# Performance work log

Hardware: AMD Instinct MI355X
Metric: run time of the kernel (lower is better)

Reference implementation:

```python
import jax, jax.numpy as jnp
import numpy as np

N_NODES = 100000
N_EDGES = 6400000
NODE_IN = 128
HID = 64


def _mlp(x, w1, b1, w2, b2):
    # Linear -> ReLU -> Linear -> ReLU
    return jax.nn.relu(jax.nn.relu(x @ w1 + b1) @ w2 + b2)


def _edge_softmax_agg(node_h, logits, src, dst, n):
    # DGL edge_softmax: softmax of edge logits over incoming edges per dst node,
    # then weighted sum of src node features scattered to dst.
    m = jax.lax.stop_gradient(jax.ops.segment_max(logits, dst, num_segments=n))
    e = jnp.exp(logits - m[dst])
    s = jax.ops.segment_sum(e, dst, num_segments=n)
    w = e / s[dst]
    return jax.ops.segment_sum(w * node_h[src], dst, num_segments=n)


def setup_inputs() -> dict:
    key = jax.random.key(0)
    ks = jax.random.split(key, 24)
    d = {
        "node_feat": jax.random.normal(ks[0], (N_NODES, NODE_IN), jnp.float32),
        "edge_feat": jax.random.normal(ks[1], (N_EDGES, 1), jnp.float32),
        "edge_dist": jax.random.normal(ks[2], (N_EDGES, 1), jnp.float32),
        "src": jax.random.randint(ks[3], (N_EDGES,), 0, N_NODES, jnp.int32),
        "dst": jax.random.randint(ks[4], (N_EDGES,), 0, N_NODES, jnp.int32),
    }
    def lin(k, fin, fout):
        kw, kb = jax.random.split(k)
        return (jax.random.normal(kw, (fin, fout), jnp.float32) / np.sqrt(fin),
                jax.random.normal(kb, (fout,), jnp.float32) * 0.01)
    d["enc_w1"], d["enc_b1"] = lin(ks[5], NODE_IN, HID)
    d["enc_w2"], d["enc_b2"] = lin(ks[6], HID, 1)
    d["nu_w1"], d["nu_b1"] = lin(ks[7], 2, HID)
    d["nu_w2"], d["nu_b2"] = lin(ks[8], HID, 1)
    d["eu_w1"], d["eu_b1"] = lin(ks[9], 3, HID)
    d["eu_w2"], d["eu_b2"] = lin(ks[10], HID, 1)
    d["dec_w1"], d["dec_b1"] = lin(ks[11], 1, HID)
    d["dec_w2"], d["dec_b2"] = lin(ks[12], HID, 1)
    return d


def reference(node_feat, edge_feat, edge_dist, src, dst,
              enc_w1, enc_b1, enc_w2, enc_b2,
              nu_w1, nu_b1, nu_w2, nu_b2,
              eu_w1, eu_b1, eu_w2, eu_b2,
              dec_w1, dec_b1, dec_w2, dec_b2):
    n = node_feat.shape[0]
    # encoder on raw node features -> [N,1]
    h = _mlp(node_feat, enc_w1, enc_b1, enc_w2, enc_b2)
    # softmax aggregation weighted by edge 'dist'
    h = _edge_softmax_agg(h, edge_dist, src, dst, n)
    # edge update: concat([edge_feat, src_h, dst_h]) -> MLP -> [E,1]
    eh = _mlp(jnp.concatenate([edge_feat, h[src], h[dst]], axis=-1),
              eu_w1, eu_b1, eu_w2, eu_b2)
    # pull: sum incoming updated edge features per dst node
    agg = jax.ops.segment_sum(eh, dst, num_segments=n)
    # node update: concat([agg_m, h]) -> MLP -> [N,1]
    h = _mlp(jnp.concatenate([agg, h], axis=-1), nu_w1, nu_b1, nu_w2, nu_b2)
    # second softmax aggregation with updated edge features as logits
    h2 = _edge_softmax_agg(h, eh, src, dst, n)
    # decoder -> [N,1]
    return _mlp(h2, dec_w1, dec_b1, dec_w2, dec_b2)
```

## Files before the change

### kernel.cpp

```cpp
#include <hip/hip_runtime.h>


#define NHB 256

typedef int   iv4 __attribute__((ext_vector_type(4)));
typedef float fv4 __attribute__((ext_vector_type(4)));
typedef float fv2 __attribute__((ext_vector_type(2)));


__global__ void __launch_bounds__(256) k_chist(
    const int* __restrict__ DST, int* __restrict__ hist,
    int e, int nbkt, int shift, int epb)
{
    __shared__ int lh[512];
    for (int c = threadIdx.x; c < nbkt; c += blockDim.x) lh[c] = 0;
    __syncthreads();
    int b = blockIdx.x;
    int i0 = b * epb, i1 = min(i0 + epb, e);
    int nq = (i1 > i0) ? ((i1 - i0) >> 2) : 0;
    const iv4* D4 = reinterpret_cast<const iv4*>(DST + i0);
    for (int q = threadIdx.x; q < nq; q += blockDim.x) {
        iv4 d = D4[q];
        atomicAdd(&lh[d.x >> shift], 1);
        atomicAdd(&lh[d.y >> shift], 1);
        atomicAdd(&lh[d.z >> shift], 1);
        atomicAdd(&lh[d.w >> shift], 1);
    }
    for (int i = i0 + 4 * nq + threadIdx.x; i < i1; i += blockDim.x)
        atomicAdd(&lh[DST[i] >> shift], 1);
    __syncthreads();
    for (int c = threadIdx.x; c < nbkt; c += blockDim.x)
        hist[(size_t)c * NHB + b] = lh[c];
}

__global__ void __launch_bounds__(256) k_scanA(
    int* __restrict__ hist, int* __restrict__ bktCnt)
{
    int c = blockIdx.x;
    int* row = hist + (size_t)c * NHB;
    __shared__ int part[256];
    int t = threadIdx.x;
    int v = row[t];
    part[t] = v;
    __syncthreads();
    for (int off = 1; off < 256; off <<= 1) {
        int x = 0;
        if (t >= off) x = part[t - off];
        __syncthreads();
        part[t] += x;
        __syncthreads();
    }
    if (t == 255) bktCnt[c] = part[255];
    row[t] = part[t] - v;
}

__global__ void __launch_bounds__(256) k_scanB(
    const int* __restrict__ bktCnt, int* __restrict__ base, int nbkt, int e)
{
    __shared__ int part[256];
    int t = threadIdx.x;
    int v[4];
    int sum = 0;
    #pragma unroll
    for (int u = 0; u < 4; ++u) {
        int idx = t * 4 + u;
        v[u] = (idx < nbkt) ? bktCnt[idx] : 0;
        sum += v[u];
    }
    part[t] = sum;
    __syncthreads();
    for (int off = 1; off < 256; off <<= 1) {
        int x = 0;
        if (t >= off) x = part[t - off];
        __syncthreads();
        part[t] += x;
        __syncthreads();
    }
    int run = (t == 0) ? 0 : part[t - 1];
    #pragma unroll
    for (int u = 0; u < 4; ++u) {
        int idx = t * 4 + u;
        if (idx < nbkt) base[idx] = run;
        run += v[u];
    }
    if (t == 0) base[nbkt] = e;
}

__global__ void __launch_bounds__(256) k_scatter(
    const int* __restrict__ DST, const int* __restrict__ SRC,
    const float* __restrict__ DIST, const float* __restrict__ EF,
    const int* __restrict__ hist, const int* __restrict__ base,
    float2* __restrict__ payA, float* __restrict__ ef_s,
    int e, int nbkt, int shift, int epb)
{
    __shared__ int loff[512];
    int b = blockIdx.x;
    for (int c = threadIdx.x; c < nbkt; c += blockDim.x)
        loff[c] = base[c] + hist[(size_t)c * NHB + b];
    __syncthreads();
    int i0 = b * epb, i1 = min(i0 + epb, e);
    if (i0 >= i1) return;
    int mask = (1 << shift) - 1;
    int nq = (i1 - i0) >> 2;
    const iv4* D4 = reinterpret_cast<const iv4*>(DST + i0);
    const iv4* S4 = reinterpret_cast<const iv4*>(SRC + i0);
    const fv4* T4 = reinterpret_cast<const fv4*>(DIST + i0);
    const fv4* F4 = reinterpret_cast<const fv4*>(EF + i0);
    for (int q = threadIdx.x; q < nq; q += blockDim.x) {
        iv4 dv = __builtin_nontemporal_load(D4 + q);
        iv4 sv = __builtin_nontemporal_load(S4 + q);
        fv4 tv = __builtin_nontemporal_load(T4 + q);
        fv4 fv = __builtin_nontemporal_load(F4 + q);
        #pragma unroll
        for (int u = 0; u < 4; ++u) {
            int d = dv[u];
            int c = d >> shift;
            int pos = atomicAdd(&loff[c], 1);
            int sd = (sv[u] << shift) | (d & mask);
            payA[pos] = make_float2(__int_as_float(sd), tv[u]);
            ef_s[pos] = fv[u];
        }
    }
    for (int i = i0 + 4 * nq + threadIdx.x; i < i1; i += blockDim.x) {
        int d = DST[i];
        int c = d >> shift;
        int pos = atomicAdd(&loff[c], 1);
        int sd = (SRC[i] << shift) | (d & mask);
        payA[pos] = make_float2(__int_as_float(sd), DIST[i]);
        ef_s[pos] = EF[i];
    }
}


__global__ void __launch_bounds__(256) k_enc(
    const float* __restrict__ X, const float* __restrict__ W1,
    const float* __restrict__ B1, const float* __restrict__ W2,
    const float* __restrict__ B2, float* __restrict__ H0, int n)
{
    __shared__ float4 w1s[2048];
    for (int t = threadIdx.x; t < 2048; t += blockDim.x)
        w1s[t] = reinterpret_cast<const float4*>(W1)[t];
    __syncthreads();

    int i = blockIdx.x * blockDim.x + threadIdx.x;
    if (i >= n) return;

    const float4* xp = reinterpret_cast<const float4*>(X) + (size_t)i * 32;

    float acc[64];
    #pragma unroll
    for (int j = 0; j < 64; ++j) acc[j] = B1[j];

    for (int k4 = 0; k4 < 32; ++k4) {
        float4 xv = xp[k4];
        #pragma unroll
        for (int kk = 0; kk < 4; ++kk) {
            float x = (&xv.x)[kk];
            const float4* wrow = &w1s[(k4 * 4 + kk) * 16];
            #pragma unroll
            for (int j4 = 0; j4 < 16; ++j4) {
                float4 w = wrow[j4];
                acc[j4*4+0] = fmaf(x, w.x, acc[j4*4+0]);
                acc[j4*4+1] = fmaf(x, w.y, acc[j4*4+1]);
                acc[j4*4+2] = fmaf(x, w.z, acc[j4*4+2]);
                acc[j4*4+3] = fmaf(x, w.w, acc[j4*4+3]);
            }
        }
    }
    float o = B2[0];
    #pragma unroll
    for (int j = 0; j < 64; ++j)
        o = fmaf(fmaxf(acc[j], 0.f), W2[j], o);
    H0[i] = fmaxf(o, 0.f);
}


__global__ void __launch_bounds__(256) k_passA(
    const float2* __restrict__ payA, const float* __restrict__ H0,
    const int* __restrict__ base,
    float* __restrict__ pSum, float* __restrict__ pNum, int shift, int G)
{
    __shared__ float lsum[512], lnum[512];
    int c = blockIdx.x / G, g = blockIdx.x % G;
    int bw = 1 << shift, mask = bw - 1;
    for (int t = threadIdx.x; t < bw; t += blockDim.x) { lsum[t] = 0.f; lnum[t] = 0.f; }
    __syncthreads();
    int b0 = base[c], len = base[c + 1] - b0;
    int i0 = b0 + (int)(((long long)len * g) / G);
    int i1 = b0 + (int)(((long long)len * (g + 1)) / G);
    for (int i = i0 + threadIdx.x; i < i1; i += blockDim.x) {
        fv2 pa = __builtin_nontemporal_load(
            reinterpret_cast<const fv2*>(payA) + i);
        int sd = __float_as_int(pa.x);
        float ev = __expf(pa.y);
        atomicAdd(&lsum[sd & mask], ev);
        atomicAdd(&lnum[sd & mask], ev * H0[sd >> shift]);
    }
    __syncthreads();
    size_t po = (size_t)blockIdx.x << shift;
    for (int t = threadIdx.x; t < bw; t += blockDim.x) {
        pSum[po + t] = lsum[t];
        pNum[po + t] = lnum[t];
    }
}

__global__ void __launch_bounds__(256) k_finA(
    const float* __restrict__ pSum, const float* __restrict__ pNum,
    float* __restrict__ H1, int shift, int n, int G)
{
    int d = blockIdx.x * blockDim.x + threadIdx.x;
    if (d >= n) return;
    int c = d >> shift, t = d & ((1 << shift) - 1);
    size_t b = (size_t)c * G << shift;
    int bw = 1 << shift;
    float s = 0.f, m = 0.f;
    for (int g = 0; g < G; ++g) {
        s += pSum[b + (size_t)g * bw + t];
        m += pNum[b + (size_t)g * bw + t];
    }
    H1[d] = (s != 0.f) ? m / s : 0.f;
}

__global__ void __launch_bounds__(256) k_passB(
    const float2* __restrict__ payA, float* __restrict__ ef_s,
    const float* __restrict__ H1,
    const float* __restrict__ W1, const float* __restrict__ B1,
    const float* __restrict__ W2, const float* __restrict__ B2,
    const int* __restrict__ base,
    float* __restrict__ pAgg, float* __restrict__ pS2, int shift, int n, int G)
{
    __shared__ float h1loc[512], lagg[512], ls2[512];
    int bw = 1 << shift, mask = bw - 1;
    int c = blockIdx.x / G, g = blockIdx.x % G;
    int d0 = c << shift;
    for (int t = threadIdx.x; t < bw; t += blockDim.x) {
        int d = d0 + t;
        h1loc[t] = (d < n) ? H1[d] : 0.f;
        lagg[t] = 0.f;
        ls2[t] = 0.f;
    }
    __syncthreads();
    const float b2 = B2[0];
    int b0 = base[c], len = base[c + 1] - b0;
    int i0 = b0 + (int)(((long long)len * g) / G);
    int i1 = b0 + (int)(((long long)len * (g + 1)) / G);
    const int T = blockDim.x;
    for (int i = i0 + (int)threadIdx.x; i < i1; i += 4 * T) {
        float x0[4], hs[4], hd[4], o[4];
        int lo[4], pos[4];
        bool val[4];
        #pragma unroll
        for (int u = 0; u < 4; ++u) {
            int j = i + u * T;
            val[u] = (j < i1);
            pos[u] = j;
            if (val[u]) {
                fv2 pa = __builtin_nontemporal_load(
                    reinterpret_cast<const fv2*>(payA) + j);
                int sd = __float_as_int(pa.x);
                lo[u] = sd & mask;
                x0[u] = __builtin_nontemporal_load(ef_s + j);
                hs[u] = H1[sd >> shift];
                hd[u] = h1loc[lo[u]];
            } else { lo[u] = 0; x0[u] = 0.f; hs[u] = 0.f; hd[u] = 0.f; }
            o[u] = b2;
        }
        #pragma unroll 4
        for (int j = 0; j < 64; ++j) {
            float aj = W1[j], bj = W1[64 + j], cj = W1[128 + j];
            float dj = B1[j], vj = W2[j];
            #pragma unroll
            for (int u = 0; u < 4; ++u) {
                float t0 = fmaf(x0[u], aj, fmaf(hs[u], bj, fmaf(hd[u], cj, dj)));
                o[u] = fmaf(fmaxf(t0, 0.f), vj, o[u]);
            }
        }
        #pragma unroll
        for (int u = 0; u < 4; ++u) {
            if (val[u]) {
                float eh = fmaxf(o[u], 0.f);
                float ex = __expf(eh);
                ef_s[pos[u]] = ex;
                atomicAdd(&lagg[lo[u]], eh);
                atomicAdd(&ls2[lo[u]], ex);
            }
        }
    }
    __syncthreads();
    size_t po = (size_t)blockIdx.x << shift;
    for (int t = threadIdx.x; t < bw; t += blockDim.x) {
        pAgg[po + t] = lagg[t];
        pS2[po + t] = ls2[t];
    }
}

__global__ void __launch_bounds__(256) k_finB(
    const float* __restrict__ pAgg, const float* __restrict__ pS2,
    const float* __restrict__ H1,
    const float* __restrict__ NW1, const float* __restrict__ NB1,
    const float* __restrict__ NW2, const float* __restrict__ NB2,
    float* __restrict__ H2, float* __restrict__ S2, int shift, int n, int G)
{
    int d = blockIdx.x * blockDim.x + threadIdx.x;
    if (d >= n) return;
    int c = d >> shift, t = d & ((1 << shift) - 1);
    size_t b = (size_t)c * G << shift;
    int bw = 1 << shift;
    float agg = 0.f, s2 = 0.f;
    for (int g = 0; g < G; ++g) {
        agg += pAgg[b + (size_t)g * bw + t];
        s2  += pS2[b + (size_t)g * bw + t];
    }
    float xh = H1[d];
    float o = NB2[0];
    #pragma unroll 4
    for (int j = 0; j < 64; ++j) {
        float a = fmaf(agg, NW1[j], fmaf(xh, NW1[64 + j], NB1[j]));
        o = fmaf(fmaxf(a, 0.f), NW2[j], o);
    }
    H2[d] = fmaxf(o, 0.f);
    S2[d] = s2;
}

__global__ void __launch_bounds__(256) k_passC(
    const float2* __restrict__ payA, const float* __restrict__ e2_s,
    const float* __restrict__ H2, const int* __restrict__ base,
    float* __restrict__ pNum, int shift, int G)
{
    __shared__ float lnum[512];
    int c = blockIdx.x / G, g = blockIdx.x % G;
    int bw = 1 << shift, mask = bw - 1;
    for (int t = threadIdx.x; t < bw; t += blockDim.x) lnum[t] = 0.f;
    __syncthreads();
    int b0 = base[c], len = base[c + 1] - b0;
    int i0 = b0 + (int)(((long long)len * g) / G);
    int i1 = b0 + (int)(((long long)len * (g + 1)) / G);
    for (int i = i0 + threadIdx.x; i < i1; i += blockDim.x) {
        fv2 pa = __builtin_nontemporal_load(
            reinterpret_cast<const fv2*>(payA) + i);
        int sd = __float_as_int(pa.x);
        float e2 = __builtin_nontemporal_load(e2_s + i);
        atomicAdd(&lnum[sd & mask], e2 * H2[sd >> shift]);
    }
    __syncthreads();
    size_t po = (size_t)blockIdx.x << shift;
    for (int t = threadIdx.x; t < bw; t += blockDim.x)
        pNum[po + t] = lnum[t];
}

__global__ void __launch_bounds__(256) k_finC(
    const float* __restrict__ pNum, const float* __restrict__ S2,
    const float* __restrict__ W1, const float* __restrict__ B1,
    const float* __restrict__ W2, const float* __restrict__ B2,
    float* __restrict__ OUT, int shift, int n, int G)
{
    int d = blockIdx.x * blockDim.x + threadIdx.x;
    if (d >= n) return;
    int c = d >> shift, t = d & ((1 << shift) - 1);
    size_t b = (size_t)c * G << shift;
    int bw = 1 << shift;
    float m = 0.f;
    for (int g = 0; g < G; ++g) m += pNum[b + (size_t)g * bw + t];
    float s = S2[d];
    float x = (s != 0.f) ? m / s : 0.f;
    float o = B2[0];
    #pragma unroll 4
    for (int j = 0; j < 64; ++j) {
        float a = fmaf(x, W1[j], B1[j]);
        o = fmaf(fmaxf(a, 0.f), W2[j], o);
    }
    OUT[d] = fmaxf(o, 0.f);
}


__device__ __forceinline__ void atomAddF(float* p, float v) { unsafeAtomicAdd(p, v); }

__global__ void k_zero(float* __restrict__ p, int n) {
    int i = blockIdx.x * blockDim.x + threadIdx.x;
    if (i < n) p[i] = 0.f;
}

__global__ void __launch_bounds__(256) k_agg1(
    const float* __restrict__ DIST, const int* __restrict__ SRC,
    const int* __restrict__ DST, const float* __restrict__ H0,
    float* __restrict__ S1, float* __restrict__ NUM1, int e)
{
    int i = blockIdx.x * blockDim.x + threadIdx.x;
    if (i >= e) return;
    float ev = __expf(DIST[i]);
    atomAddF(&S1[DST[i]], ev);
    atomAddF(&NUM1[DST[i]], ev * H0[SRC[i]]);
}

__global__ void k_div(const float* __restrict__ NUM, const float* __restrict__ S,
                      float* __restrict__ H, int n) {
    int i = blockIdx.x * blockDim.x + threadIdx.x;
    if (i < n) {
        float s = S[i];
        H[i] = (s != 0.f) ? NUM[i] / s : 0.f;
    }
}

__global__ void __launch_bounds__(256) k_edgeF(
    const float* __restrict__ EF, const int* __restrict__ SRC,
    const int* __restrict__ DST, const float* __restrict__ H1,
    const float* __restrict__ W1, const float* __restrict__ B1,
    const float* __restrict__ W2, const float* __restrict__ B2,
    float* __restrict__ E2, float* __restrict__ AGG, float* __restrict__ S2, int e)
{
    int i = blockIdx.x * blockDim.x + threadIdx.x;
    if (i >= e) return;
    float x0 = EF[i];
    int s = SRC[i], d = DST[i];
    float h_s = H1[s], h_d = H1[d];
    float o = B2[0];
    for (int j = 0; j < 64; ++j) {
        float aj = fmaf(x0, W1[j], fmaf(h_s, W1[64+j], fmaf(h_d, W1[128+j], B1[j])));
        o = fmaf(fmaxf(aj, 0.f), W2[j], o);
    }
    float eh = fmaxf(o, 0.f);
    float ex = __expf(eh);
    E2[i] = ex;
    atomAddF(&AGG[d], eh);
    atomAddF(&S2[d], ex);
}

__global__ void k_nu(const float* __restrict__ AGG, const float* __restrict__ H1,
                     const float* __restrict__ W1, const float* __restrict__ B1,
                     const float* __restrict__ W2, const float* __restrict__ B2,
                     float* __restrict__ H2, int n)
{
    int i = blockIdx.x * blockDim.x + threadIdx.x;
    if (i >= n) return;
    float x0 = AGG[i], x1 = H1[i];
    float o = B2[0];
    #pragma unroll
    for (int j = 0; j < 64; ++j) {
        float a = fmaf(x0, W1[j], fmaf(x1, W1[64 + j], B1[j]));
        o = fmaf(fmaxf(a, 0.f), W2[j], o);
    }
    H2[i] = fmaxf(o, 0.f);
}

__global__ void __launch_bounds__(256) k_agg2F(
    const float* __restrict__ E2, const int* __restrict__ SRC,
    const int* __restrict__ DST, const float* __restrict__ H2,
    float* __restrict__ NUM2, int e)
{
    int i = blockIdx.x * blockDim.x + threadIdx.x;
    if (i >= e) return;
    atomAddF(&NUM2[DST[i]], E2[i] * H2[SRC[i]]);
}

__global__ void k_final(const float* __restrict__ NUM2, const float* __restrict__ S2,
                        const float* __restrict__ W1, const float* __restrict__ B1,
                        const float* __restrict__ W2, const float* __restrict__ B2,
                        float* __restrict__ OUT, int n)
{
    int i = blockIdx.x * blockDim.x + threadIdx.x;
    if (i >= n) return;
    float s = S2[i];
    float x = (s != 0.f) ? NUM2[i] / s : 0.f;
    float o = B2[0];
    #pragma unroll
    for (int j = 0; j < 64; ++j) {
        float a = fmaf(x, W1[j], B1[j]);
        o = fmaf(fmaxf(a, 0.f), W2[j], o);
    }
    OUT[i] = fmaxf(o, 0.f);
}


extern "C" void kernel_launch(void* const* d_in, const int* in_sizes, int n_in,
                              void* d_out, int out_size, void* d_ws, size_t ws_size,
                              hipStream_t stream)
{
    const float* node_feat = (const float*)d_in[0];
    const float* edge_feat = (const float*)d_in[1];
    const float* edge_dist = (const float*)d_in[2];
    const int*   src       = (const int*)d_in[3];
    const int*   dst       = (const int*)d_in[4];
    const float* enc_w1 = (const float*)d_in[5];
    const float* enc_b1 = (const float*)d_in[6];
    const float* enc_w2 = (const float*)d_in[7];
    const float* enc_b2 = (const float*)d_in[8];
    const float* nu_w1  = (const float*)d_in[9];
    const float* nu_b1  = (const float*)d_in[10];
    const float* nu_w2  = (const float*)d_in[11];
    const float* nu_b2  = (const float*)d_in[12];
    const float* eu_w1  = (const float*)d_in[13];
    const float* eu_b1  = (const float*)d_in[14];
    const float* eu_w2  = (const float*)d_in[15];
    const float* eu_b2  = (const float*)d_in[16];
    const float* dec_w1 = (const float*)d_in[17];
    const float* dec_b1 = (const float*)d_in[18];
    const float* dec_w2 = (const float*)d_in[19];
    const float* dec_b2 = (const float*)d_in[20];

    const int n = in_sizes[0] / 128;
    const int e = in_sizes[1];
    const int B = 256;

    int shift = 9;
    while ((((n + (1 << shift) - 1) >> shift) > 512) && shift < 12) shift++;
    const int nbkt = (n + (1 << shift) - 1) >> shift;
    int epb = (e + NHB - 1) / NHB;
    epb = (epb + 3) & ~3;

    float* ws = (float*)d_ws;
    size_t w = (size_t)4 * n;
    int* base   = (int*)(ws + w); w += nbkt + 1;
    int* bktCnt = (int*)(ws + w); w += nbkt;
    int* hist   = (int*)(ws + w); w += (size_t)nbkt * NHB;
    w = (w + 1) & ~(size_t)1;
    float2* payA = (float2*)(ws + w); w += (size_t)2 * e;
    float* ef_s  = ws + w; w += e;

    int G = 8;
    size_t psz;
    size_t need;
    for (;;) {
        psz = ((size_t)nbkt * G) << shift;
        need = (w + 2 * psz) * 4;
        if (need <= ws_size || G == 1) break;
        G >>= 1;
    }
    float* pP0 = ws + w;
    float* pP1 = ws + w + psz;

    float* h0 = ws;
    float* h1 = ws + (size_t)1 * n;
    float* h2 = ws + (size_t)2 * n;
    float* s2 = ws + (size_t)3 * n;

    if (ws_size >= need && nbkt <= 512 && (1 << shift) <= 512 &&
        ((size_t)n << shift) < (1u << 30)) {
        const int gE = nbkt * G;
        hipLaunchKernelGGL(k_chist, dim3(NHB), dim3(B), 0, stream,
                           dst, hist, e, nbkt, shift, epb);
        hipLaunchKernelGGL(k_scanA, dim3(nbkt), dim3(B), 0, stream, hist, bktCnt);
        hipLaunchKernelGGL(k_scanB, dim3(1), dim3(B), 0, stream, bktCnt, base, nbkt, e);
        hipLaunchKernelGGL(k_scatter, dim3(NHB), dim3(B), 0, stream,
                           dst, src, edge_dist, edge_feat, hist, base,
                           payA, ef_s, e, nbkt, shift, epb);
        hipLaunchKernelGGL(k_enc, dim3((n + B - 1) / B), dim3(B), 0, stream,
                           node_feat, enc_w1, enc_b1, enc_w2, enc_b2, h0, n);
        hipLaunchKernelGGL(k_passA, dim3(gE), dim3(B), 0, stream,
                           payA, h0, base, pP0, pP1, shift, G);
        hipLaunchKernelGGL(k_finA, dim3((n + B - 1) / B), dim3(B), 0, stream,
                           pP0, pP1, h1, shift, n, G);
        hipLaunchKernelGGL(k_passB, dim3(gE), dim3(B), 0, stream,
                           payA, ef_s, h1, eu_w1, eu_b1, eu_w2, eu_b2, base,
                           pP0, pP1, shift, n, G);
        hipLaunchKernelGGL(k_finB, dim3((n + B - 1) / B), dim3(B), 0, stream,
                           pP0, pP1, h1, nu_w1, nu_b1, nu_w2, nu_b2, h2, s2,
                           shift, n, G);
        hipLaunchKernelGGL(k_passC, dim3(gE), dim3(B), 0, stream,
                           payA, ef_s , h2, base, pP0, shift, G);
        hipLaunchKernelGGL(k_finC, dim3((n + B - 1) / B), dim3(B), 0, stream,
                           pP0, s2, dec_w1, dec_b1, dec_w2, dec_b2,
                           (float*)d_out, shift, n, G);
    } else {
        float* agg  = ws + (size_t)2 * n;
        float* s1   = ws + (size_t)4 * n;
        float* num1 = ws + (size_t)5 * n;
        float* num2 = ws + (size_t)6 * n;
        float* h2f  = ws + (size_t)7 * n;
        float* e2   = ws + (size_t)8 * n;
        hipLaunchKernelGGL(k_zero, dim3((5 * n + B - 1) / B), dim3(B), 0, stream,
                           agg, 5 * n);
        hipLaunchKernelGGL(k_enc, dim3((n + B - 1) / B), dim3(B), 0, stream,
                           node_feat, enc_w1, enc_b1, enc_w2, enc_b2, h0, n);
        hipLaunchKernelGGL(k_agg1, dim3((e + B - 1) / B), dim3(B), 0, stream,
                           edge_dist, src, dst, h0, s1, num1, e);
        hipLaunchKernelGGL(k_div, dim3((n + B - 1) / B), dim3(B), 0, stream,
                           num1, s1, h1, n);
        hipLaunchKernelGGL(k_edgeF, dim3((e + B - 1) / B), dim3(B), 0, stream,
                           edge_feat, src, dst, h1, eu_w1, eu_b1, eu_w2, eu_b2,
                           e2, agg, s2, e);
        hipLaunchKernelGGL(k_nu, dim3((n + B - 1) / B), dim3(B), 0, stream,
                           agg, h1, nu_w1, nu_b1, nu_w2, nu_b2, h2f, n);
        hipLaunchKernelGGL(k_agg2F, dim3((e + B - 1) / B), dim3(B), 0, stream,
                           e2, src, dst, h2f, num2, e);
        hipLaunchKernelGGL(k_final, dim3((n + B - 1) / B), dim3(B), 0, stream,
                           num2, s2, dec_w1, dec_b1, dec_w2, dec_b2, (float*)d_out, n);
    }
}
```

Before: 402.4 us.

## Unroll edge passes, prefetch payloads in passB, use packed FMA, raise G

passA and passC now process two edges per iteration so more gathers are in flight at once. passB software-pipelines its loads by fetching the next group of four edges' payloads before computing the current group. Its 64-wide hidden MLP now uses two-lane packed FMA/max, which can map to packed-float instructions on CDNA. The number of blocks per bucket grows from 8 to 16. This raises parallelism but also raises register pressure and the partial-buffer size and reduction cost, and summing the two lanes changes floating-point summation order.

```diff
diff --git a/kernel.cpp b/kernel.cpp
--- a/kernel.cpp
+++ b/kernel.cpp
@@ -6,6 +6,21 @@
 typedef int   iv4 __attribute__((ext_vector_type(4)));
 typedef float fv4 __attribute__((ext_vector_type(4)));
 typedef float fv2 __attribute__((ext_vector_type(2)));
+
+#if __has_builtin(__builtin_elementwise_fma)
+#define FMA2(a, b, c) __builtin_elementwise_fma((a), (b), (c))
+#else
+static __device__ __forceinline__ fv2 FMA2(fv2 a, fv2 b, fv2 c) {
+    fv2 r; r.x = fmaf(a.x, b.x, c.x); r.y = fmaf(a.y, b.y, c.y); return r;
+}
+#endif
+#if __has_builtin(__builtin_elementwise_max)
+#define MAX2(a, b) __builtin_elementwise_max((a), (b))
+#else
+static __device__ __forceinline__ fv2 MAX2(fv2 a, fv2 b) {
+    fv2 r; r.x = fmaxf(a.x, b.x); r.y = fmaxf(a.y, b.y); return r;
+}
+#endif
 
 
 __global__ void __launch_bounds__(256) k_chist(
@@ -188,13 +203,27 @@
     int b0 = base[c], len = base[c + 1] - b0;
     int i0 = b0 + (int)(((long long)len * g) / G);
     int i1 = b0 + (int)(((long long)len * (g + 1)) / G);
-    for (int i = i0 + threadIdx.x; i < i1; i += blockDim.x) {
-        fv2 pa = __builtin_nontemporal_load(
+    const int T = blockDim.x;
+    for (int i = i0 + (int)threadIdx.x; i < i1; i += 2 * T) {
+        int jb = i + T;
+        fv2 p0 = __builtin_nontemporal_load(
             reinterpret_cast<const fv2*>(payA) + i);
-        int sd = __float_as_int(pa.x);
-        float ev = __expf(pa.y);
-        atomicAdd(&lsum[sd & mask], ev);
-        atomicAdd(&lnum[sd & mask], ev * H0[sd >> shift]);
+        fv2 p1 = {0.f, 0.f};
+        bool vb = jb < i1;
+        if (vb) p1 = __builtin_nontemporal_load(
+                    reinterpret_cast<const fv2*>(payA) + jb);
+        int sd0 = __float_as_int(p0.x);
+        int sd1 = __float_as_int(p1.x);
+        float h0a = H0[sd0 >> shift];
+        float h0b = vb ? H0[sd1 >> shift] : 0.f;
+        float e0 = __expf(p0.y);
+        float e1 = __expf(p1.y);
+        atomicAdd(&lsum[sd0 & mask], e0);
+        atomicAdd(&lnum[sd0 & mask], e0 * h0a);
+        if (vb) {
+            atomicAdd(&lsum[sd1 & mask], e1);
+            atomicAdd(&lnum[sd1 & mask], e1 * h0b);
+        }
     }
     __syncthreads();
     size_t po = (size_t)blockIdx.x << shift;
@@ -230,6 +259,7 @@
     float* __restrict__ pAgg, float* __restrict__ pS2, int shift, int n, int G)
 {
     __shared__ float h1loc[512], lagg[512], ls2[512];
+    const fv2 ZERO2 = {0.f, 0.f};
     int bw = 1 << shift, mask = bw - 1;
     int c = blockIdx.x / G, g = blockIdx.x % G;
     int d0 = c << shift;
@@ -245,46 +275,77 @@
     int i0 = b0 + (int)(((long long)len * g) / G);
     int i1 = b0 + (int)(((long long)len * (g + 1)) / G);
     const int T = blockDim.x;
-    for (int i = i0 + (int)threadIdx.x; i < i1; i += 4 * T) {
-        float x0[4], hs[4], hd[4], o[4];
-        int lo[4], pos[4];
-        bool val[4];
+
+    int i = i0 + (int)threadIdx.x;
+    fv2 pa[4]; float xf[4];
+    #pragma unroll
+    for (int u = 0; u < 4; ++u) {
+        int j = i + u * T;
+        pa[u] = ZERO2; xf[u] = 0.f;
+        if (j < i1) {
+            pa[u] = __builtin_nontemporal_load(
+                reinterpret_cast<const fv2*>(payA) + j);
+            xf[u] = __builtin_nontemporal_load(ef_s + j);
+        }
+    }
+    while (i < i1) {
+        int inext = i + 4 * T;
+        fv2 pb[4]; float xg[4];
+        #pragma unroll
+        for (int u = 0; u < 4; ++u) {
+            int j = inext + u * T;
+            pb[u] = ZERO2; xg[u] = 0.f;
+            if (j < i1) {
+                pb[u] = __builtin_nontemporal_load(
+                    reinterpret_cast<const fv2*>(payA) + j);
+                xg[u] = __builtin_nontemporal_load(ef_s + j);
+            }
+        }
+        fv2 x0v[4], hsv[4], hdv[4], o2[4];
+        int lo[4];
+        #pragma unroll
+        for (int u = 0; u < 4; ++u) {
+            int sd = __float_as_int(pa[u].x);
+            lo[u] = sd & mask;
+            float hs = H1[sd >> shift];
+            float hd = h1loc[lo[u]];
+            fv2 xt; xt.x = xf[u]; xt.y = xf[u];
+            x0v[u] = xt;
+            fv2 ht; ht.x = hs; ht.y = hs;
+            hsv[u] = ht;
+            fv2 dt; dt.x = hd; dt.y = hd;
+            hdv[u] = dt;
+            o2[u] = ZERO2;
+        }
+        #pragma unroll 4
+        for (int j = 0; j < 64; j += 2) {
+            fv2 aj = *reinterpret_cast<const fv2*>(W1 + j);
+            fv2 bj = *reinterpret_cast<const fv2*>(W1 + 64 + j);
+            fv2 cj = *reinterpret_cast<const fv2*>(W1 + 128 + j);
+            fv2 dj = *reinterpret_cast<const fv2*>(B1 + j);
+            fv2 vj = *reinterpret_cast<const fv2*>(W2 + j);
+            #pragma unroll
+            for (int u = 0; u < 4; ++u) {
+                fv2 t = FMA2(x0v[u], aj,
+                         FMA2(hsv[u], bj, FMA2(hdv[u], cj, dj)));
+                t = MAX2(t, ZERO2);
+                o2[u] = FMA2(t, vj, o2[u]);
+            }
+        }
         #pragma unroll
         for (int u = 0; u < 4; ++u) {
             int j = i + u * T;
-            val[u] = (j < i1);
-            pos[u] = j;
-            if (val[u]) {
-                fv2 pa = __builtin_nontemporal_load(
-                    reinterpret_cast<const fv2*>(payA) + j);
-                int sd = __float_as_int(pa.x);
-                lo[u] = sd & mask;
-                x0[u] = __builtin_nontemporal_load(ef_s + j);
-                hs[u] = H1[sd >> shift];
-                hd[u] = h1loc[lo[u]];
-            } else { lo[u] = 0; x0[u] = 0.f; hs[u] = 0.f; hd[u] = 0.f; }
-            o[u] = b2;
-        }
-        #pragma unroll 4
-        for (int j = 0; j < 64; ++j) {
-            float aj = W1[j], bj = W1[64 + j], cj = W1[128 + j];
-            float dj = B1[j], vj = W2[j];
-            #pragma unroll
-            for (int u = 0; u < 4; ++u) {
-                float t0 = fmaf(x0[u], aj, fmaf(hs[u], bj, fmaf(hd[u], cj, dj)));
-                o[u] = fmaf(fmaxf(t0, 0.f), vj, o[u]);
-            }
-        }
-        #pragma unroll
-        for (int u = 0; u < 4; ++u) {
-            if (val[u]) {
-                float eh = fmaxf(o[u], 0.f);
+            if (j < i1) {
+                float eh = fmaxf(o2[u].x + o2[u].y + b2, 0.f);
                 float ex = __expf(eh);
-                ef_s[pos[u]] = ex;
+                ef_s[j] = ex;
                 atomicAdd(&lagg[lo[u]], eh);
                 atomicAdd(&ls2[lo[u]], ex);
             }
         }
+        i = inext;
+        #pragma unroll
+        for (int u = 0; u < 4; ++u) { pa[u] = pb[u]; xf[u] = xg[u]; }
     }
     __syncthreads();
     size_t po = (size_t)blockIdx.x << shift;
@@ -335,12 +396,26 @@
     int b0 = base[c], len = base[c + 1] - b0;
     int i0 = b0 + (int)(((long long)len * g) / G);
     int i1 = b0 + (int)(((long long)len * (g + 1)) / G);
-    for (int i = i0 + threadIdx.x; i < i1; i += blockDim.x) {
-        fv2 pa = __builtin_nontemporal_load(
+    const int T = blockDim.x;
+    for (int i = i0 + (int)threadIdx.x; i < i1; i += 2 * T) {
+        int jb = i + T;
+        bool vb = jb < i1;
+        fv2 p0 = __builtin_nontemporal_load(
             reinterpret_cast<const fv2*>(payA) + i);
-        int sd = __float_as_int(pa.x);
-        float e2 = __builtin_nontemporal_load(e2_s + i);
-        atomicAdd(&lnum[sd & mask], e2 * H2[sd >> shift]);
+        float e0 = __builtin_nontemporal_load(e2_s + i);
+        fv2 p1 = {0.f, 0.f};
+        float e1 = 0.f;
+        if (vb) {
+            p1 = __builtin_nontemporal_load(
+                reinterpret_cast<const fv2*>(payA) + jb);
+            e1 = __builtin_nontemporal_load(e2_s + jb);
+        }
+        int sd0 = __float_as_int(p0.x);
+        int sd1 = __float_as_int(p1.x);
+        float m0 = e0 * H2[sd0 >> shift];
+        float m1 = vb ? e1 * H2[sd1 >> shift] : 0.f;
+        atomicAdd(&lnum[sd0 & mask], m0);
+        if (vb) atomicAdd(&lnum[sd1 & mask], m1);
     }
     __syncthreads();
     size_t po = (size_t)blockIdx.x << shift;
@@ -516,7 +591,7 @@
     float2* payA = (float2*)(ws + w); w += (size_t)2 * e;
     float* ef_s  = ws + w; w += e;
 
-    int G = 8;
+    int G = 16;
     size_t psz;
     size_t need;
     for (;;) {
```

Result: no change. 397.5 us (-1.2%).
